# Kernel optimization log

Hardware: AMD Instinct MI355X
Metric: run time of the kernel (lower is better)

Reference implementation:

```python
import jax, jax.numpy as jnp
import numpy as np

N_QUERIES = 33_554_432  # 32M query points (128 MB fp32)
N_KNOTS = 1024          # interpolation table size


def setup_inputs() -> dict:
    key = jax.random.key(0)
    k1, k2, k3 = jax.random.split(key, 3)
    # queries spread slightly beyond the knot range to exercise clamping branches
    x = jax.random.uniform(k1, (N_QUERIES,), dtype=jnp.float32, minval=-0.1, maxval=1.1)
    # unsorted knots (module sorts them in __init__; reference sorts too)
    x_points = jax.random.uniform(k2, (N_KNOTS,), dtype=jnp.float32)
    y_points = jax.random.normal(k3, (N_KNOTS,), dtype=jnp.float32)
    return {"x": x, "x_points": x_points, "y_points": y_points}


def reference(x, x_points, y_points):
    # __init__: sort knots by x, permute y accordingly
    order = jnp.argsort(x_points)
    xp = x_points[order]
    yp = y_points[order]
    n = xp.shape[0]
    # torch.searchsorted default (right=False) == side='left'
    idx = jnp.searchsorted(xp, x, side="left")  # [N], int
    # interior lerp uses (idx-1, idx); clip so gathers are in-range
    hi = jnp.clip(idx, 1, n - 1)
    lo = hi - 1
    x1, x2 = xp[lo], xp[hi]
    y1, y2 = yp[lo], yp[hi]
    interp = y1 + (x - x1) * (y2 - y1) / (x2 - x1)
    # boundary clamps: idx==0 -> y[0]; idx>=n -> y[-1]
    out = jnp.where(idx == 0, yp[0], jnp.where(idx >= n, yp[-1], interp))
    return out
```

## Files before the change

### kernel.cpp

```cpp
#include <hip/hip_runtime.h>
#include <math.h>

#define NK 1024
#define NB 4096

#define WS_QUAD_OFF 1028
#define WS_TAB_OFF  (1028 + 4096)

__device__ __forceinline__ int bucket_of(float x, float lo, float scale) {
    float t = __fmul_rn(__fsub_rn(x, lo), scale);
    int b = (int)t;
    b = b < 0 ? 0 : b;
    b = b > (NB - 1) ? (NB - 1) : b;
    return b;
}

__global__ __launch_bounds__(1024) void setup_kernel(
        const float* __restrict__ xp_in, const float* __restrict__ yp_in,
        float* __restrict__ wsf)
{
    __shared__ float2 kv[NK];
    __shared__ float2 kv2[NK];
    __shared__ int    hist[NB];
    __shared__ int    starts[NB];
    __shared__ int    iscan[NK];
    __shared__ float  red[NK];
    __shared__ int    flag;
    __shared__ float  s_lo, s_scale;

    const int t = threadIdx.x;
    float xv = xp_in[t];
    kv[t] = make_float2(xv, yp_in[t]);

    red[t] = xv; __syncthreads();
    for (int s = 512; s > 0; s >>= 1) {
        if (t < s) red[t] = fminf(red[t], red[t + s]);
        __syncthreads();
    }
    if (t == 0) s_lo = red[0];
    __syncthreads();
    red[t] = xv; __syncthreads();
    for (int s = 512; s > 0; s >>= 1) {
        if (t < s) red[t] = fmaxf(red[t], red[t + s]);
        __syncthreads();
    }
    if (t == 0) {
        float range = red[0] - s_lo;
        s_scale = (range > 0.0f) ? ((float)NB / range) : 0.0f;
    }
    __syncthreads();
    const float lo = s_lo, scale = s_scale;

    for (int i = t; i < NB; i += NK) hist[i] = 0;
    __syncthreads();
    const int bt = bucket_of(xv, lo, scale);
    atomicAdd(&hist[bt], 1);
    __syncthreads();

    int c0 = hist[4 * t], c1 = hist[4 * t + 1], c2 = hist[4 * t + 2], c3 = hist[4 * t + 3];
    int tot = c0 + c1 + c2 + c3;
    iscan[t] = tot; __syncthreads();
    for (int off = 1; off < NK; off <<= 1) {
        int v = (t >= off) ? iscan[t - off] : 0;
        __syncthreads();
        iscan[t] += v;
        __syncthreads();
    }
    int excl = iscan[t] - tot;
    starts[4 * t]     = excl;
    starts[4 * t + 1] = excl + c0;
    starts[4 * t + 2] = excl + c0 + c1;
    starts[4 * t + 3] = excl + c0 + c1 + c2;
    __syncthreads();

    for (int i = t; i < NB; i += NK) hist[i] = 0;
    __syncthreads();
    int pos = starts[bt] + atomicAdd(&hist[bt], 1);
    kv2[pos] = kv[t];
    __syncthreads();

    for (;;) {
        if (t == 0) flag = 0;
        __syncthreads();
        if (t < NK / 2) {
            int i0 = 2 * t;
            float2 a = kv2[i0], b = kv2[i0 + 1];
            if (a.x > b.x) { kv2[i0] = b; kv2[i0 + 1] = a; flag = 1; }
        }
        __syncthreads();
        if (t < NK / 2 - 1) {
            int i0 = 2 * t + 1;
            float2 a = kv2[i0], b = kv2[i0 + 1];
            if (a.x > b.x) { kv2[i0] = b; kv2[i0 + 1] = a; flag = 1; }
        }
        __syncthreads();
        if (!flag) break;
    }

    wsf[t] = kv2[t].x;
    if (t == 0) {
        wsf[NK]   = INFINITY;
        wsf[1025] = lo;
        wsf[1026] = scale;
    }
    float2 cur = kv2[t];
    float2 nxt = kv2[(t == NK - 1) ? (NK - 1) : (t + 1)];
    float4* qg = (float4*)(wsf + WS_QUAD_OFF);
    qg[t] = make_float4(cur.x, cur.y, nxt.x, nxt.y);
    unsigned short* tg = (unsigned short*)(wsf + WS_TAB_OFF);
    tg[4 * t]     = (unsigned short)starts[4 * t];
    tg[4 * t + 1] = (unsigned short)starts[4 * t + 1];
    tg[4 * t + 2] = (unsigned short)starts[4 * t + 2];
    tg[4 * t + 3] = (unsigned short)starts[4 * t + 3];
}

__device__ __forceinline__ float interp_one(
        float x, const float* __restrict__ sxp, const float4* __restrict__ quads,
        const unsigned short* __restrict__ table,
        float lo, float scale, float xp0, float xpN, float yp0, float ypN)
{
    int b = bucket_of(x, lo, scale);
    int j = table[b];
    while (sxp[j] < x) ++j;
    int hi = j < 1 ? 1 : (j > NK - 1 ? NK - 1 : j);
    float4 qd = quads[hi - 1];
    float r = __builtin_amdgcn_rcpf(qd.z - qd.x);
    float res = qd.y + (x - qd.x) * (qd.w - qd.y) * r;
    res = (x <= xp0) ? yp0 : res;
    res = (x >  xpN) ? ypN : res;
    return res;
}

__global__ __launch_bounds__(256, 4) void interp_kernel(
        const float4* __restrict__ xq, float4* __restrict__ out,
        const float* __restrict__ wsf, int n4)
{
    __shared__ float          sxp[NK + 1];
    __shared__ float4         quads[NK];
    __shared__ unsigned short table[NB];

    const int t = threadIdx.x;
    for (int i = t; i < NK + 1; i += 256) sxp[i] = wsf[i];
    const float lo = wsf[1025], scale = wsf[1026];
    const float4* qsrc = (const float4*)(wsf + WS_QUAD_OFF);
    for (int i = t; i < NK; i += 256) quads[i] = qsrc[i];
    const unsigned int* tsrc = (const unsigned int*)(wsf + WS_TAB_OFF);
    unsigned int* tdst = (unsigned int*)table;
    for (int i = t; i < NB / 2; i += 256) tdst[i] = tsrc[i];
    __syncthreads();

    const float xp0 = sxp[0], xpN = sxp[NK - 1];
    const float yp0 = quads[0].y, ypN = quads[NK - 1].y;

    int idx = blockIdx.x * 256 + t;
    const int stride = gridDim.x * 256;
    for (int q = idx; q < n4; q += stride) {
        float4 xv = xq[q];
        float4 r;
        r.x = interp_one(xv.x, sxp, quads, table, lo, scale, xp0, xpN, yp0, ypN);
        r.y = interp_one(xv.y, sxp, quads, table, lo, scale, xp0, xpN, yp0, ypN);
        r.z = interp_one(xv.z, sxp, quads, table, lo, scale, xp0, xpN, yp0, ypN);
        r.w = interp_one(xv.w, sxp, quads, table, lo, scale, xp0, xpN, yp0, ypN);
        out[q] = r;
    }
}

extern "C" void kernel_launch(void* const* d_in, const int* in_sizes, int n_in,
                              void* d_out, int out_size, void* d_ws, size_t ws_size,
                              hipStream_t stream)
{
    const float* x  = (const float*)d_in[0];
    const float* xp = (const float*)d_in[1];
    const float* yp = (const float*)d_in[2];
    float* out = (float*)d_out;
    float* wsf = (float*)d_ws;

    setup_kernel<<<1, 1024, 0, stream>>>(xp, yp, wsf);

    const int n4 = out_size / 4;
    interp_kernel<<<1280, 256, 0, stream>>>((const float4*)x, (float4*)out, wsf, n4);
}
```

Before: 240.3 us.

## Precompute per-bucket lerp records and move knot search to global memory

Halves the bucket count and has setup emit one float4 record per bucket. Empty buckets store a precomputed base point and slope, so their queries finish with a single FMA. Non-empty buckets store a start index, and their queries fall back to a linear search over knots and quads read from global memory rather than LDS. The interp kernel now stages only the record table in shared memory, uses nontemporal vector loads and stores, and asks for higher occupancy. The risk is wavefront divergence: a wave runs the slow path whenever any of its 64 lanes hits a non-empty bucket, and that path now pays global or cache latency instead of LDS latency.

```diff
diff --git a/kernel.cpp b/kernel.cpp
--- a/kernel.cpp
+++ b/kernel.cpp
@@ -2,10 +2,12 @@
 #include <math.h>
 
 #define NK 1024
-#define NB 4096
+#define NB 2048
+
+typedef float f32x4 __attribute__((ext_vector_type(4)));
 
 #define WS_QUAD_OFF 1028
-#define WS_TAB_OFF  (1028 + 4096)
+#define WS_REC_OFF  5124
 
 __device__ __forceinline__ int bucket_of(float x, float lo, float scale) {
     float t = __fmul_rn(__fsub_rn(x, lo), scale);
@@ -51,14 +53,14 @@
     __syncthreads();
     const float lo = s_lo, scale = s_scale;
 
-    for (int i = t; i < NB; i += NK) hist[i] = 0;
+    for (int i = t; i < NB; i += 1024) hist[i] = 0;
     __syncthreads();
     const int bt = bucket_of(xv, lo, scale);
     atomicAdd(&hist[bt], 1);
     __syncthreads();
 
-    int c0 = hist[4 * t], c1 = hist[4 * t + 1], c2 = hist[4 * t + 2], c3 = hist[4 * t + 3];
-    int tot = c0 + c1 + c2 + c3;
+    int c0 = hist[2 * t], c1 = hist[2 * t + 1];
+    int tot = c0 + c1;
     iscan[t] = tot; __syncthreads();
     for (int off = 1; off < NK; off <<= 1) {
         int v = (t >= off) ? iscan[t - off] : 0;
@@ -67,13 +69,11 @@
         __syncthreads();
     }
     int excl = iscan[t] - tot;
-    starts[4 * t]     = excl;
-    starts[4 * t + 1] = excl + c0;
-    starts[4 * t + 2] = excl + c0 + c1;
-    starts[4 * t + 3] = excl + c0 + c1 + c2;
+    starts[2 * t]     = excl;
+    starts[2 * t + 1] = excl + c0;
     __syncthreads();
 
-    for (int i = t; i < NB; i += NK) hist[i] = 0;
+    for (int i = t; i < NB; i += 1024) hist[i] = 0;
     __syncthreads();
     int pos = starts[bt] + atomicAdd(&hist[bt], 1);
     kv2[pos] = kv[t];
@@ -107,61 +107,72 @@
     float2 nxt = kv2[(t == NK - 1) ? (NK - 1) : (t + 1)];
     float4* qg = (float4*)(wsf + WS_QUAD_OFF);
     qg[t] = make_float4(cur.x, cur.y, nxt.x, nxt.y);
-    unsigned short* tg = (unsigned short*)(wsf + WS_TAB_OFF);
-    tg[4 * t]     = (unsigned short)starts[4 * t];
-    tg[4 * t + 1] = (unsigned short)starts[4 * t + 1];
-    tg[4 * t + 2] = (unsigned short)starts[4 * t + 2];
-    tg[4 * t + 3] = (unsigned short)starts[4 * t + 3];
+
+    float4* rg = (float4*)(wsf + WS_REC_OFF);
+    for (int b = t; b < NB; b += 1024) {
+        int cnt = hist[b];
+        int st  = starts[b];
+        float4 rec;
+        if (cnt == 0) {
+            int hi = st < 1 ? 1 : (st > NK - 1 ? NK - 1 : st);
+            float2 p1 = kv2[hi - 1];
+            float2 p2 = kv2[hi];
+            float slope = (p2.y - p1.y) / (p2.x - p1.x);
+            rec = make_float4(p1.x, p1.y, slope, __int_as_float(-1));
+        } else {
+            rec = make_float4(0.0f, 0.0f, 0.0f, __int_as_float(st));
+        }
+        rg[b] = rec;
+    }
 }
 
-__device__ __forceinline__ float interp_one(
-        float x, const float* __restrict__ sxp, const float4* __restrict__ quads,
-        const unsigned short* __restrict__ table,
-        float lo, float scale, float xp0, float xpN, float yp0, float ypN)
-{
-    int b = bucket_of(x, lo, scale);
-    int j = table[b];
-    while (sxp[j] < x) ++j;
-    int hi = j < 1 ? 1 : (j > NK - 1 ? NK - 1 : j);
-    float4 qd = quads[hi - 1];
-    float r = __builtin_amdgcn_rcpf(qd.z - qd.x);
-    float res = qd.y + (x - qd.x) * (qd.w - qd.y) * r;
-    res = (x <= xp0) ? yp0 : res;
-    res = (x >  xpN) ? ypN : res;
-    return res;
-}
-
-__global__ __launch_bounds__(256, 4) void interp_kernel(
-        const float4* __restrict__ xq, float4* __restrict__ out,
+__global__ __launch_bounds__(256, 5) void interp_kernel(
+        const f32x4* __restrict__ xq, f32x4* __restrict__ out,
         const float* __restrict__ wsf, int n4)
 {
-    __shared__ float          sxp[NK + 1];
-    __shared__ float4         quads[NK];
-    __shared__ unsigned short table[NB];
+    __shared__ float4 recs[NB];
 
     const int t = threadIdx.x;
-    for (int i = t; i < NK + 1; i += 256) sxp[i] = wsf[i];
-    const float lo = wsf[1025], scale = wsf[1026];
-    const float4* qsrc = (const float4*)(wsf + WS_QUAD_OFF);
-    for (int i = t; i < NK; i += 256) quads[i] = qsrc[i];
-    const unsigned int* tsrc = (const unsigned int*)(wsf + WS_TAB_OFF);
-    unsigned int* tdst = (unsigned int*)table;
-    for (int i = t; i < NB / 2; i += 256) tdst[i] = tsrc[i];
+    const float lo    = wsf[1025];
+    const float scale = wsf[1026];
+    const float xp0   = wsf[0];
+    const float xpN   = wsf[NK - 1];
+    const float yp0   = wsf[WS_QUAD_OFF + 1];
+    const float ypN   = wsf[WS_QUAD_OFF + 4 * (NK - 1) + 1];
+    const float*  gsxp   = wsf;
+    const float4* gquads = (const float4*)(wsf + WS_QUAD_OFF);
+
+    const float4* rsrc = (const float4*)(wsf + WS_REC_OFF);
+    for (int i = t; i < NB; i += 256) recs[i] = rsrc[i];
     __syncthreads();
-
-    const float xp0 = sxp[0], xpN = sxp[NK - 1];
-    const float yp0 = quads[0].y, ypN = quads[NK - 1].y;
 
     int idx = blockIdx.x * 256 + t;
     const int stride = gridDim.x * 256;
     for (int q = idx; q < n4; q += stride) {
-        float4 xv = xq[q];
-        float4 r;
-        r.x = interp_one(xv.x, sxp, quads, table, lo, scale, xp0, xpN, yp0, ypN);
-        r.y = interp_one(xv.y, sxp, quads, table, lo, scale, xp0, xpN, yp0, ypN);
-        r.z = interp_one(xv.z, sxp, quads, table, lo, scale, xp0, xpN, yp0, ypN);
-        r.w = interp_one(xv.w, sxp, quads, table, lo, scale, xp0, xpN, yp0, ypN);
-        out[q] = r;
+        f32x4 xv = __builtin_nontemporal_load(&xq[q]);
+        float xs[4] = {xv.x, xv.y, xv.z, xv.w};
+        float rs[4];
+#pragma unroll
+        for (int c = 0; c < 4; ++c) {
+            float x = xs[c];
+            int b = bucket_of(x, lo, scale);
+            float4 rec = recs[b];
+            float res = fmaf(x - rec.x, rec.z, rec.y);
+            int w = __float_as_int(rec.w);
+            if (w >= 0) {
+                int j = w;
+                while (gsxp[j] < x) ++j;
+                int hi = j < 1 ? 1 : (j > NK - 1 ? NK - 1 : j);
+                float4 qd = gquads[hi - 1];
+                float r = __builtin_amdgcn_rcpf(qd.z - qd.x);
+                res = qd.y + (x - qd.x) * (qd.w - qd.y) * r;
+                res = (x <= xp0) ? yp0 : res;
+                res = (x >  xpN) ? ypN : res;
+            }
+            rs[c] = res;
+        }
+        f32x4 r4 = {rs[0], rs[1], rs[2], rs[3]};
+        __builtin_nontemporal_store(r4, &out[q]);
     }
 }
 
@@ -178,5 +189,5 @@
     setup_kernel<<<1, 1024, 0, stream>>>(xp, yp, wsf);
 
     const int n4 = out_size / 4;
-    interp_kernel<<<1280, 256, 0, stream>>>((const float4*)x, (float4*)out, wsf, n4);
+    interp_kernel<<<1280, 256, 0, stream>>>((const f32x4*)x, (f32x4*)out, wsf, n4);
 }
```

Measured after the change: 430.5 us. 79.2% more time.
